# Kernel optimization log

Measured on AMD Instinct MI355X. Metric: run time of the kernel, lower is better.

Reference implementation:

```python
import jax, jax.numpy as jnp
import numpy as np

B, T, D = 16, 512, 384
MAX_MEL = 4096  # static upper bound = T * max_duration(8)


def setup_inputs() -> dict:
    key = jax.random.key(0)
    k1, k2, k3 = jax.random.split(key, 3)
    batch = jax.random.normal(k1, (B, T, D), dtype=jnp.float32)
    token_lengths = jax.random.randint(k2, (B,), 1, T + 1).astype(jnp.int64)
    token_durations = jax.random.randint(k3, (B, T), 0, 8).astype(jnp.int32)
    return {"batch": batch, "token_lengths": token_lengths,
            "token_durations": token_durations, "alpha": 1}


def reference(batch, token_lengths, token_durations, alpha):
    # alpha == 1.0 default path: durations used as-is (ceil of ints is identity).
    durs = token_durations.astype(jnp.int32)
    if alpha != 1.0:
        durs = jnp.round(durs.astype(jnp.float32) * alpha).astype(jnp.int32)
    # mask tokens beyond each example's length (equivalent to slicing token[:len])
    tok_mask = jnp.arange(T)[None, :] < token_lengths[:, None]   # [B, T]
    durs = jnp.where(tok_mask, durs, 0)
    csum = jnp.cumsum(durs, axis=1)                               # [B, T] cumulative end offsets
    mel_lens = csum[:, -1]                                        # [B]

    # For each output frame t, source token = first j with csum[j] > t
    frames = jnp.arange(MAX_MEL, dtype=jnp.int32)                 # [MAX_MEL]
    idx = jax.vmap(lambda c: jnp.searchsorted(c, frames, side='right'))(csum)  # [B, MAX_MEL]
    idx = jnp.clip(idx, 0, T - 1)
    out = jnp.take_along_axis(batch, idx[:, :, None], axis=1)     # [B, MAX_MEL, D]

    valid = frames[None, :] < mel_lens[:, None]                   # zero-pad past mel_len
    out = out * valid[:, :, None].astype(out.dtype)
    return out, mel_lens.astype(jnp.float32)
```

## Files before the change

### kernel.cpp

```cpp
#include <hip/hip_runtime.h>

#define NB   16
#define NT   512
#define ND   384
#define NMEL 4096
#define ROWV (ND / 4)
#define BPB  128
#define FPB  (NMEL / BPB)
#define NTHR 256
#define VPT  ((FPB * ROWV) / NTHR)
#define GRP  6

typedef float f32x4 __attribute__((ext_vector_type(4)));

__global__ __launch_bounds__(NTHR) void dr_fused_kernel(
    const f32x4* __restrict__ batch,
    const int*   __restrict__ tl32,
    const int2*  __restrict__ td2,
    const int*   __restrict__ alpha_ptr,
    f32x4*       __restrict__ out,
    float*       __restrict__ mel_lens)
{
    const int b     = blockIdx.x >> 7;
    const int chunk = blockIdx.x & (BPB - 1);
    const int t     = threadIdx.x;
    const int lane  = t & 63;
    const int w     = t >> 6;

    __shared__ int scsum[NT];
    __shared__ int wtot[4];
    __shared__ int s_idx[FPB];

    bool is64 = true;
    #pragma unroll
    for (int i = 1; i < NB; i += 2) {
        if (tl32[i] != 0) is64 = false;
    }
    const int len = is64 ? tl32[2 * b] : tl32[b];

    const int   araw  = alpha_ptr[0];
    const float abits = __int_as_float(araw);
    const bool  alpha_one = (araw == 1) || (abits == 1.0f);

    const int i0 = 2 * t, i1 = 2 * t + 1;
    int2 dd = td2[b * (NT / 2) + t];
    int d0 = dd.x, d1 = dd.y;
    if (!alpha_one) {
        float a = (abits > 0.001f && abits < 1000.0f) ? abits : (float)araw;
        d0 = (int)rintf((float)d0 * a);
        d1 = (int)rintf((float)d1 * a);
    }
    if (i0 >= len) d0 = 0;
    if (i1 >= len) d1 = 0;

    int sc = d0 + d1;
    #pragma unroll
    for (int off = 1; off < 64; off <<= 1) {
        int v = __shfl_up(sc, off, 64);
        if (lane >= off) sc += v;
    }
    if (lane == 63) wtot[w] = sc;
    __syncthreads();

    int woff = 0, total = 0;
    #pragma unroll
    for (int j = 0; j < 4; ++j) {
        const int wv = wtot[j];
        total += wv;
        if (j < w) woff += wv;
    }
    const int S = sc + woff;
    scsum[i1] = S;
    scsum[i0] = S - d1;
    __syncthreads();

    if (chunk == 0 && t == 0) mel_lens[b] = (float)total;

    const int f0 = chunk * FPB;
    if (t < FPB) {
        const int f = f0 + t;
        int lo = 0, hi = NT;
        while (lo < hi) {
            const int mid = (lo + hi) >> 1;
            if (scsum[mid] <= f) lo = mid + 1; else hi = mid;
        }
        int idx = (lo < NT) ? lo : (NT - 1);
        s_idx[t] = (f < total) ? idx : -1;
    }
    __syncthreads();

    const f32x4* brow = batch + (size_t)b * NT * ROWV;
    f32x4*       orow = out + ((size_t)b * NMEL + f0) * ROWV;
    #pragma unroll
    for (int g = 0; g < VPT / GRP; ++g) {
        int   ee[GRP];
        f32x4 v[GRP];
        #pragma unroll
        for (int i = 0; i < GRP; ++i) {
            const int e   = t + (g * GRP + i) * NTHR;
            const int fl  = e / ROWV;
            const int col = e - fl * ROWV;
            const int enc = s_idx[fl];
            const int rc  = (enc >= 0 ? enc : 0) * ROWV + col;
            f32x4 vv = brow[rc];
            v[i]  = (enc >= 0) ? vv : (f32x4)(0.f);
            ee[i] = e;
        }
        #pragma unroll
        for (int i = 0; i < GRP; ++i) {
            orow[ee[i]] = v[i];
        }
    }
}

extern "C" void kernel_launch(void* const* d_in, const int* in_sizes, int n_in,
                              void* d_out, int out_size, void* d_ws, size_t ws_size,
                              hipStream_t stream) {
    const float* batch = (const float*)d_in[0];
    const int*   tl    = (const int*)d_in[1];
    const int*   td    = (const int*)d_in[2];
    const int*   alpha = (const int*)d_in[3];

    float* out      = (float*)d_out;
    float* mel_lens = out + (size_t)NB * NMEL * ND;

    dr_fused_kernel<<<NB * BPB, NTHR, 0, stream>>>(
        (const f32x4*)batch, tl, (const int2*)td, alpha, (f32x4*)out, mel_lens);
}
```

Baseline: 22.08 us.

## Scatter token indices directly and interleave frame chunks across blocks

Each block now owns frames chunk, chunk+128, ... (strided) instead of a contiguous range, so every thread scatters its two tokens' frame ranges straight into the shared index table. This removes the shared cumsum array, one barrier and the per-frame binary search. Loads for frames past the mel length are skipped using a per-block valid-frame count. The cost is that output rows are written with a 128-row stride rather than contiguously, and frames past the last token but below total are no longer clamped as before (that case cannot occur here).

Measured after the change: 22.52 us. Within noise of the previous version (+2.0%).

```diff
diff --git a/kernel.cpp b/kernel.cpp
--- a/kernel.cpp
+++ b/kernel.cpp
@@ -27,7 +27,6 @@
     const int lane  = t & 63;
     const int w     = t >> 6;
 
-    __shared__ int scsum[NT];
     __shared__ int wtot[4];
     __shared__ int s_idx[FPB];
 
@@ -70,27 +69,31 @@
         if (j < w) woff += wv;
     }
     const int S = sc + woff;
-    scsum[i1] = S;
-    scsum[i0] = S - d1;
-    __syncthreads();
 
     if (chunk == 0 && t == 0) mel_lens[b] = (float)total;
 
-    const int f0 = chunk * FPB;
-    if (t < FPB) {
-        const int f = f0 + t;
-        int lo = 0, hi = NT;
-        while (lo < hi) {
-            const int mid = (lo + hi) >> 1;
-            if (scsum[mid] <= f) lo = mid + 1; else hi = mid;
-        }
-        int idx = (lo < NT) ? lo : (NT - 1);
-        s_idx[t] = (f < total) ? idx : -1;
+    {
+        int lo1 = S - d1, hi1 = S;
+        int lo0 = lo1 - d0, hi0 = lo1;
+        int a0 = lo0 - chunk, c0 = hi0 - chunk;
+        int a1 = lo1 - chunk, c1 = hi1 - chunk;
+        int k0 = (a0 <= 0) ? 0 : ((a0 + BPB - 1) >> 7);
+        int k0e = (c0 <= 0) ? 0 : ((c0 + BPB - 1) >> 7);
+        if (k0e > FPB) k0e = FPB;
+        for (int k = k0; k < k0e; ++k) s_idx[k] = i0;
+        int k1 = (a1 <= 0) ? 0 : ((a1 + BPB - 1) >> 7);
+        int k1e = (c1 <= 0) ? 0 : ((c1 + BPB - 1) >> 7);
+        if (k1e > FPB) k1e = FPB;
+        for (int k = k1; k < k1e; ++k) s_idx[k] = i1;
     }
     __syncthreads();
 
+    const int tc = total - chunk;
+    const int nvalid = (tc <= 0) ? 0 : min(FPB, (tc + BPB - 1) >> 7);
+    const int vlimit = nvalid * ROWV;
+
     const f32x4* brow = batch + (size_t)b * NT * ROWV;
-    f32x4*       orow = out + ((size_t)b * NMEL + f0) * ROWV;
+    f32x4*       ob   = out + ((size_t)b * NMEL + chunk) * ROWV;
     #pragma unroll
     for (int g = 0; g < VPT / GRP; ++g) {
         int   ee[GRP];
@@ -100,15 +103,17 @@
             const int e   = t + (g * GRP + i) * NTHR;
             const int fl  = e / ROWV;
             const int col = e - fl * ROWV;
-            const int enc = s_idx[fl];
-            const int rc  = (enc >= 0 ? enc : 0) * ROWV + col;
-            f32x4 vv = brow[rc];
-            v[i]  = (enc >= 0) ? vv : (f32x4)(0.f);
-            ee[i] = e;
+            f32x4 vv = (f32x4)(0.f);
+            if (e < vlimit) {
+                const int enc = s_idx[fl];
+                vv = brow[enc * ROWV + col];
+            }
+            v[i]  = vv;
+            ee[i] = fl * (BPB * ROWV) + col;
         }
         #pragma unroll
         for (int i = 0; i < GRP; ++i) {
-            orow[ee[i]] = v[i];
+            ob[ee[i]] = v[i];
         }
     }
 }
```
